# Kernel optimization log

Measured on AMD Instinct MI355X. Metric: run time of the kernel, lower is better.

The kernel has to match this reference:

```python
import jax, jax.numpy as jnp
import numpy as np

BN_EPS = 1e-5


def _maxpool2(x):
    # x: [b, c, h, w] -> [b, c, h//2, w//2], 2x2 max pool, stride 2
    b, c, h, w = x.shape
    return x.reshape(b, c, h // 2, 2, w // 2, 2).max(axis=(3, 5))


def setup_inputs() -> dict:
    key = jax.random.key(0)
    ks = jax.random.split(key, 9)
    b, C, H, W = 8, 512, 64, 64
    Ci = C // 2  # inter_channels = 256
    return {
        "x": jax.random.normal(ks[0], (b, C, H, W), dtype=jnp.float32),
        "g_w": jax.random.normal(ks[1], (Ci, C), dtype=jnp.float32) * 0.02,
        "g_b": jax.random.normal(ks[2], (Ci,), dtype=jnp.float32) * 0.02,
        "W_w": jax.random.normal(ks[3], (C, Ci), dtype=jnp.float32) * 0.02,
        "W_b": jax.random.normal(ks[4], (C,), dtype=jnp.float32) * 0.02,
        "bn_gamma": jax.random.normal(ks[5], (C,), dtype=jnp.float32),
        "bn_beta": jax.random.normal(ks[6], (C,), dtype=jnp.float32),
        "bn_mean": jax.random.normal(ks[7], (C,), dtype=jnp.float32),
        "bn_var": jax.random.uniform(ks[8], (C,), dtype=jnp.float32, minval=0.5, maxval=1.5),
    }


def reference(x, g_w, g_b, W_w, W_b, bn_gamma, bn_beta, bn_mean, bn_var):
    b, C, H, W = x.shape
    Ci = g_w.shape[0]

    # g branch: conv1x1 (C -> Ci) then 2x2 maxpool, flatten to values [b, Nk, Ci]
    g_x = jnp.einsum('bchw,oc->bohw', x, g_w) + g_b[None, :, None, None]
    g_x = _maxpool2(g_x).reshape(b, Ci, -1).transpose(0, 2, 1)  # [b, Nk, Ci]

    # theta: identity, flattened queries [b, Nq, C]
    theta = x.reshape(b, C, -1).transpose(0, 2, 1)  # [b, Nq, C]
    # phi: identity + 2x2 maxpool, keys [b, C, Nk]
    phi = _maxpool2(x).reshape(b, C, -1)  # [b, C, Nk]

    # attention (unscaled dot product + softmax over keys)
    f = jnp.einsum('bnc,bck->bnk', theta, phi)  # [b, Nq, Nk]
    attn = jax.nn.softmax(f, axis=-1)
    y = jnp.einsum('bnk,bko->bno', attn, g_x)  # [b, Nq, Ci]
    y = y.transpose(0, 2, 1).reshape(b, Ci, H, W)

    # W: conv1x1 (Ci -> C) + BatchNorm2d (eval mode with running stats)
    W_y = jnp.einsum('bchw,oc->bohw', y, W_w) + W_b[None, :, None, None]
    inv_std = jax.lax.rsqrt(bn_var + BN_EPS)
    W_y = (W_y - bn_mean[None, :, None, None]) * (bn_gamma * inv_std)[None, :, None, None] \
          + bn_beta[None, :, None, None]

    return W_y + x
```

## Files before the change

kernel.cpp:

```cpp
#include <hip/hip_runtime.h>
#include <stdint.h>

typedef __attribute__((ext_vector_type(4))) float f32x4;
typedef __attribute__((ext_vector_type(8))) short short8_t;
typedef __attribute__((ext_vector_type(8))) unsigned short ushort8_t;

__device__ __forceinline__ unsigned short f2bf(float f) {
    unsigned int u = __builtin_bit_cast(unsigned int, f);
    u = (u + 0x7fffu + ((u >> 16) & 1u)) >> 16;
    return (unsigned short)u;
}
__device__ __forceinline__ float bf2f(unsigned short h) {
    unsigned int u = ((unsigned int)h) << 16;
    return __builtin_bit_cast(float, u);
}

__device__ __forceinline__ void gll16(const unsigned short* g, unsigned short* l) {
    __builtin_amdgcn_global_load_lds(
        (const __attribute__((address_space(1))) void*)g,
        (__attribute__((address_space(3))) void*)l, 16, 0, 0);
}

__global__ __launch_bounds__(256) void prep_w(
    const float* __restrict__ g_w, const float* __restrict__ W_w,
    const float* __restrict__ W_b, const float* __restrict__ gamma,
    const float* __restrict__ beta, const float* __restrict__ mean,
    const float* __restrict__ var,
    unsigned short* __restrict__ gwb, unsigned short* __restrict__ wwb,
    float* __restrict__ bnA, float* __restrict__ bnB)
{
    int i = blockIdx.x * 256 + threadIdx.x;
    if (i < 256 * 512) { gwb[i] = f2bf(g_w[i]); wwb[i] = f2bf(W_w[i]); }
    if (i < 512) {
        float is = rsqrtf(var[i] + 1e-5f);
        float a = gamma[i] * is;
        bnA[i] = a;
        bnB[i] = (W_b[i] - mean[i]) * a + beta[i];
    }
}

__global__ __launch_bounds__(256) void build_qk(
    const float* __restrict__ x, unsigned short* __restrict__ Qh,
    unsigned short* __restrict__ Kh)
{
    __shared__ float t[32][129];
    int b = blockIdx.z;
    int p0 = blockIdx.x * 128, c0 = blockIdx.y * 32;
    const float* xb = x + (long)b * 512 * 4096;
    int tid = threadIdx.x;
    for (int i = 0; i < 16; i++) {
        int idx = i * 256 + tid;
        int c = idx >> 7, p = idx & 127;
        t[c][p] = xb[(long)(c0 + c) * 4096 + p0 + p];
    }
    __syncthreads();
    unsigned short* qb = Qh + (long)b * 4096 * 512;
    for (int i = 0; i < 16; i++) {
        int idx = i * 256 + tid;
        int p = idx >> 5, c = idx & 31;
        qb[(long)(p0 + p) * 512 + c0 + c] = f2bf(t[c][p]);
    }
    unsigned short* kb = Kh + (long)b * 1024 * 512;
    int kp0 = p0 >> 2;
    for (int i = 0; i < 4; i++) {
        int idx = i * 256 + tid;
        int w = idx >> 5, c = idx & 31;
        float v = fmaxf(fmaxf(t[c][2 * w], t[c][2 * w + 1]),
                        fmaxf(t[c][64 + 2 * w], t[c][64 + 2 * w + 1]));
        kb[(long)(kp0 + w) * 512 + c0 + c] = f2bf(v);
    }
}

__global__ __launch_bounds__(256) void build_v(
    const unsigned short* __restrict__ Gt, const float* __restrict__ g_b,
    unsigned short* __restrict__ Gp)
{
    int b = blockIdx.z;
    int k  = blockIdx.x * 32 + (threadIdx.x & 31);
    int ci = blockIdx.y * 8 + (threadIdx.x >> 5);
    int h = k >> 5, w = k & 31;
    const unsigned short* g = Gt + (long)b * 4096 * 256;
    long p = (long)(h * 128 + w * 2) * 256 + ci;
    float v0 = bf2f(g[p]),        v1 = bf2f(g[p + 256]);
    float v2 = bf2f(g[p + 64*256]), v3 = bf2f(g[p + 65*256]);
    float v = fmaxf(fmaxf(v0, v1), fmaxf(v2, v3)) + g_b[ci];
    Gp[(long)b * 256 * 1024 + (long)ci * 1024 + k] = f2bf(v);
}

__global__ __launch_bounds__(256) void smax_rows(
    const unsigned short* __restrict__ S, float* __restrict__ Smax)
{
    long row = (long)blockIdx.x * 4 + (threadIdx.x >> 6);
    int lane = threadIdx.x & 63;
    const unsigned short* r = S + row * 1024 + lane * 16;
    ushort8_t v0 = *(const ushort8_t*)r;
    ushort8_t v1 = *(const ushort8_t*)(r + 8);
    float m = -3.0e38f;
    for (int e = 0; e < 8; e++) m = fmaxf(m, fmaxf(bf2f(v0[e]), bf2f(v1[e])));
    for (int off = 32; off; off >>= 1) m = fmaxf(m, __shfl_xor(m, off));
    if (lane == 0) Smax[row] = m;
}

__global__ __launch_bounds__(256) void pv_fused(
    const unsigned short* __restrict__ S, long sbstr,
    const float* __restrict__ Smax, long mxstr,
    const unsigned short* __restrict__ Gp, long gbstr,
    unsigned short* __restrict__ Y, long ybstr)
{
    __shared__ unsigned short lV[256 * 64];
    __shared__ unsigned short lP[64 * 64];
    __shared__ float li[64];

    const int tid = threadIdx.x;
    const int wid = tid >> 6, lane = tid & 63;

    unsigned gx = gridDim.x, gy = gridDim.y;
    unsigned nwg = gx * gy;
    unsigned lin = blockIdx.x + gx * blockIdx.y;
    unsigned l = ((nwg & 7u) == 0u) ? ((lin & 7u) * (nwg >> 3) + (lin >> 3)) : lin;
    unsigned bx = l % gx, by = l / gx;

    const int q0 = (int)bx * 64;
    const unsigned short* Sb = S + by * sbstr + (long)q0 * 1024;
    const unsigned short* Gb = Gp + by * gbstr;
    unsigned short* Yb = Y + by * ybstr + (long)q0 * 256;

    const int wr = wid >> 1, wc = wid & 1;
    const int lr = lane & 15, lg = lane >> 4;
    const int srA = lane >> 3;
    const int scg = (((lane & 7) ^ srA) << 3);
    const int pr = tid >> 2;
    const int pc = (tid & 3) * 2;

    const float m = Smax[by * mxstr + q0 + pr];

    f32x4 acc[2][8];
    for (int mi = 0; mi < 2; mi++)
        for (int ni = 0; ni < 8; ni++)
            acc[mi][ni] = (f32x4){0.f, 0.f, 0.f, 0.f};
    float psum = 0.f;

    for (int kb = 0; kb < 16; kb++) {
        __syncthreads();
        for (int i = 0; i < 8; i++) {
            int cibase = i * 32 + wid * 8;
            gll16(Gb + (long)(cibase + srA) * 1024 + kb * 64 + scg, &lV[cibase * 64]);
        }
        {
            const unsigned short* sp = Sb + (long)pr * 1024 + kb * 64 + pc * 8;
            for (int j = 0; j < 2; j++) {
                ushort8_t v = *(const ushort8_t*)(sp + j * 8);
                ushort8_t o8;
                for (int e = 0; e < 8; e++) {
                    float pe = __expf(bf2f(v[e]) - m);
                    psum += pe;
                    o8[e] = f2bf(pe);
                }
                int c = pc + j;
                *(ushort8_t*)(&lP[pr * 64 + ((c ^ (pr & 7)) * 8)]) = o8;
            }
        }
        __syncthreads();
        for (int ks = 0; ks < 2; ks++) {
            short8_t af[2], bfr[8];
            for (int mi = 0; mi < 2; mi++) {
                int row = wr * 32 + mi * 16 + lr;
                int ch = ((ks * 4 + lg) ^ (row & 7)) * 8;
                af[mi] = *(const short8_t*)(&lP[row * 64 + ch]);
            }
            for (int ni = 0; ni < 8; ni++) {
                int row = wc * 128 + ni * 16 + lr;
                int ch = ((ks * 4 + lg) ^ (row & 7)) * 8;
                bfr[ni] = *(const short8_t*)(&lV[row * 64 + ch]);
            }
            for (int mi = 0; mi < 2; mi++)
                for (int ni = 0; ni < 8; ni++)
                    acc[mi][ni] = __builtin_amdgcn_mfma_f32_16x16x32_bf16(
                        af[mi], bfr[ni], acc[mi][ni], 0, 0, 0);
        }
    }

    psum += __shfl_xor(psum, 1);
    psum += __shfl_xor(psum, 2);
    if ((tid & 3) == 0) li[pr] = 1.0f / psum;
    __syncthreads();

    for (int mi = 0; mi < 2; mi++) {
        for (int ni = 0; ni < 8; ni++) {
            int ci = wc * 128 + ni * 16 + lr;
            int rbase = wr * 32 + mi * 16 + lg * 4;
            for (int r = 0; r < 4; r++) {
                int row = rbase + r;
                Yb[(long)row * 256 + ci] = f2bf(acc[mi][ni][r] * li[row]);
            }
        }
    }
}

template<int EPI>
__global__ __launch_bounds__(256) void gemm_abt(
    const unsigned short* __restrict__ A, int lda, long abstr,
    const unsigned short* __restrict__ B, int ldb, long bbstr,
    void* __restrict__ Cv, int ldc, long cbstr,
    int K,
    const float* __restrict__ bnA, const float* __restrict__ bnB,
    const float* __restrict__ Xres, long xbstr)
{
    __shared__ unsigned short lA[128 * 64];
    __shared__ unsigned short lB[128 * 64];
    const int tid = threadIdx.x;
    const int wid = tid >> 6, lane = tid & 63;

    unsigned gx = gridDim.x, gy = gridDim.y;
    unsigned nwg = gx * gy * gridDim.z;
    unsigned lin = blockIdx.x + gx * (blockIdx.y + gy * blockIdx.z);
    unsigned l = ((nwg & 7u) == 0u) ? ((lin & 7u) * (nwg >> 3) + (lin >> 3)) : lin;
    unsigned bx = l % gx;
    unsigned rem = l / gx;
    unsigned by = rem % gy;
    unsigned bz = rem / gy;

    const int z = (int)bz;
    const int m0 = (int)by * 128, n0 = (int)bx * 128;
    const unsigned short* Ab = A + z * abstr;
    const unsigned short* Bb = B + z * bbstr;
    const int wr = wid >> 1, wc = wid & 1;
    const int lr = lane & 15, lg = lane >> 4;

    const int srA = lane >> 3;
    const int scg = (((lane & 7) ^ srA) << 3);

    f32x4 acc[4][4];
    for (int mi = 0; mi < 4; mi++)
        for (int ni = 0; ni < 4; ni++)
            acc[mi][ni] = (f32x4){0.f, 0.f, 0.f, 0.f};

    for (int k0 = 0; k0 < K; k0 += 64) {
        __syncthreads();
        for (int i = 0; i < 4; i++) {
            int rowbase = i * 32 + wid * 8;
            gll16(Ab + (long)(m0 + rowbase + srA) * lda + k0 + scg, &lA[rowbase * 64]);
            gll16(Bb + (long)(n0 + rowbase + srA) * ldb + k0 + scg, &lB[rowbase * 64]);
        }
        __syncthreads();
        for (int kk = 0; kk < 2; kk++) {
            short8_t af[4], bfr[4];
            for (int mi = 0; mi < 4; mi++) {
                int row = wr * 64 + mi * 16 + lr;
                int ch = ((kk * 4 + lg) ^ (row & 7)) * 8;
                af[mi] = *(const short8_t*)(&lA[row * 64 + ch]);
            }
            for (int ni = 0; ni < 4; ni++) {
                int row = wc * 64 + ni * 16 + lr;
                int ch = ((kk * 4 + lg) ^ (row & 7)) * 8;
                bfr[ni] = *(const short8_t*)(&lB[row * 64 + ch]);
            }
            for (int mi = 0; mi < 4; mi++)
                for (int ni = 0; ni < 4; ni++)
                    acc[mi][ni] = __builtin_amdgcn_mfma_f32_16x16x32_bf16(
                        af[mi], bfr[ni], acc[mi][ni], 0, 0, 0);
        }
    }

    for (int mi = 0; mi < 4; mi++) {
        for (int ni = 0; ni < 4; ni++) {
            int ncol = n0 + wc * 64 + ni * 16 + lr;
            int mrow = m0 + wr * 64 + mi * 16 + lg * 4;
            for (int r = 0; r < 4; r++) {
                int row = mrow + r;
                float v = acc[mi][ni][r];
                long idx = z * cbstr + (long)row * ldc + ncol;
                if (EPI == 0) {
                    ((float*)Cv)[idx] = v;
                } else if (EPI == 1) {
                    ((unsigned short*)Cv)[idx] = f2bf(v);
                } else {
                    float o = v * bnA[row] + bnB[row] + Xres[z * xbstr + (long)row * ldc + ncol];
                    ((float*)Cv)[idx] = o;
                }
            }
        }
    }
}

__global__ void copy_residual(const float* __restrict__ x, float* __restrict__ out, long n)
{
    for (long i = blockIdx.x * 256ll + threadIdx.x; i < n; i += (long)gridDim.x * 256)
        out[i] = x[i];
}

extern "C" void kernel_launch(void* const* d_in, const int* in_sizes, int n_in,
                              void* d_out, int out_size, void* d_ws, size_t ws_size,
                              hipStream_t stream)
{
    const float* x     = (const float*)d_in[0];
    const float* g_w   = (const float*)d_in[1];
    const float* g_b   = (const float*)d_in[2];
    const float* W_w   = (const float*)d_in[3];
    const float* W_b   = (const float*)d_in[4];
    const float* gamma = (const float*)d_in[5];
    const float* beta  = (const float*)d_in[6];
    const float* mean  = (const float*)d_in[7];
    const float* var   = (const float*)d_in[8];
    float* out = (float*)d_out;

    char* ws = (char*)d_ws;
    size_t o = 0;
    auto alloc = [&](size_t bytes) { size_t r = o; o = (o + bytes + 255) & ~(size_t)255; return r; };
    size_t o_gwb = alloc(256 * 512 * 2);
    size_t o_wwb = alloc(512 * 256 * 2);
    size_t o_bnA = alloc(512 * 4);
    size_t o_bnB = alloc(512 * 4);
    size_t o_q   = alloc(8ull * 4096 * 512 * 2);
    size_t o_k   = alloc(8ull * 1024 * 512 * 2);
    size_t o_gp  = alloc(8ull * 256 * 1024 * 2);
    size_t o_y   = alloc(8ull * 4096 * 256 * 2);
    size_t o_m   = alloc(8ull * 4096 * 4);
    size_t o_s   = o;
    const size_t srow_bytes = 1024ull * 2;
    const size_t sb1 = 4096ull * srow_bytes;

    int G = 0, RC = 0;
    if      (o_s + 8 * sb1 <= ws_size) G = 8;
    else if (o_s + 4 * sb1 <= ws_size) G = 4;
    else if (o_s + 2 * sb1 <= ws_size) G = 2;
    else if (o_s + 1 * sb1 <= ws_size) G = 1;
    else {
        for (int rc = 2048; rc >= 128; rc >>= 1)
            if (o_s + (size_t)rc * srow_bytes <= ws_size) { RC = rc; break; }
        if (!RC) {
            copy_residual<<<dim3(2048), dim3(256), 0, stream>>>(x, out, (long)out_size);
            return;
        }
    }

    unsigned short* gwb = (unsigned short*)(ws + o_gwb);
    unsigned short* wwb = (unsigned short*)(ws + o_wwb);
    float* bnA = (float*)(ws + o_bnA);
    float* bnB = (float*)(ws + o_bnB);
    unsigned short* Qh  = (unsigned short*)(ws + o_q);
    unsigned short* Kh  = (unsigned short*)(ws + o_k);
    unsigned short* Gp  = (unsigned short*)(ws + o_gp);
    unsigned short* Y   = (unsigned short*)(ws + o_y);
    float* Smax         = (float*)(ws + o_m);
    unsigned short* S   = (unsigned short*)(ws + o_s);

    prep_w<<<dim3(512), dim3(256), 0, stream>>>(g_w, W_w, W_b, gamma, beta, mean, var,
                                                gwb, wwb, bnA, bnB);
    build_qk<<<dim3(32, 16, 8), dim3(256), 0, stream>>>(x, Qh, Kh);

    gemm_abt<1><<<dim3(2, 32, 8), dim3(256), 0, stream>>>(
        Qh, 512, 4096l * 512,
        gwb, 512, 0,
        (void*)Y, 256, 4096l * 256, 512,
        nullptr, nullptr, nullptr, 0);

    build_v<<<dim3(32, 32, 8), dim3(256), 0, stream>>>(Y, g_b, Gp);

    if (G) {
        for (int bg = 0; bg < 8; bg += G) {
            gemm_abt<1><<<dim3(8, 32, G), dim3(256), 0, stream>>>(
                Qh + (size_t)bg * 4096 * 512, 512, 4096l * 512,
                Kh + (size_t)bg * 1024 * 512, 512, 1024l * 512,
                (void*)S, 1024, 4096l * 1024, 512,
                nullptr, nullptr, nullptr, 0);
            smax_rows<<<dim3(G * 1024), dim3(256), 0, stream>>>(S, Smax);
            pv_fused<<<dim3(64, G), dim3(256), 0, stream>>>(
                S, 4096l * 1024,
                Smax, 4096,
                Gp + (size_t)bg * 256 * 1024, 256l * 1024,
                Y + (size_t)bg * 4096 * 256, 4096l * 256);
        }
    } else {
        for (int b = 0; b < 8; b++) {
            for (int r0 = 0; r0 < 4096; r0 += RC) {
                const unsigned short* Aq = Qh + (size_t)b * 4096 * 512 + (size_t)r0 * 512;
                gemm_abt<1><<<dim3(8, RC / 128, 1), dim3(256), 0, stream>>>(
                    Aq, 512, 0,
                    Kh + (size_t)b * 1024 * 512, 512, 0,
                    (void*)S, 1024, 0, 512,
                    nullptr, nullptr, nullptr, 0);
                smax_rows<<<dim3(RC / 4), dim3(256), 0, stream>>>(S, Smax);
                pv_fused<<<dim3(RC / 64, 1), dim3(256), 0, stream>>>(
                    S, 0,
                    Smax, 0,
                    Gp + (size_t)b * 256 * 1024, 0,
                    Y + ((size_t)b * 4096 + r0) * 256, 0);
            }
        }
    }

    gemm_abt<2><<<dim3(32, 4, 8), dim3(256), 0, stream>>>(
        wwb, 256, 0,
        Y, 256, 4096l * 256,
        (void*)out, 4096, 512l * 4096, 256,
        bnA, bnB, x, 512l * 4096);
}
```

Before: 178.5 us.

## Fuse g-branch conv GEMM into QK score GEMM launch and hoist S loads

```diff
diff --git a/kernel.cpp b/kernel.cpp
--- a/kernel.cpp
+++ b/kernel.cpp
@@ -142,23 +142,27 @@
 
     for (int kb = 0; kb < 16; kb++) {
         __syncthreads();
+        const unsigned short* sp = Sb + (long)pr * 1024 + kb * 64 + pc * 8;
+        ushort8_t v0 = *(const ushort8_t*)sp;
+        ushort8_t v1 = *(const ushort8_t*)(sp + 8);
         for (int i = 0; i < 8; i++) {
             int cibase = i * 32 + wid * 8;
             gll16(Gb + (long)(cibase + srA) * 1024 + kb * 64 + scg, &lV[cibase * 64]);
         }
         {
-            const unsigned short* sp = Sb + (long)pr * 1024 + kb * 64 + pc * 8;
-            for (int j = 0; j < 2; j++) {
-                ushort8_t v = *(const ushort8_t*)(sp + j * 8);
-                ushort8_t o8;
-                for (int e = 0; e < 8; e++) {
-                    float pe = __expf(bf2f(v[e]) - m);
-                    psum += pe;
-                    o8[e] = f2bf(pe);
-                }
-                int c = pc + j;
-                *(ushort8_t*)(&lP[pr * 64 + ((c ^ (pr & 7)) * 8)]) = o8;
-            }
+            ushort8_t o8;
+            for (int e = 0; e < 8; e++) {
+                float pe = __expf(bf2f(v0[e]) - m);
+                psum += pe;
+                o8[e] = f2bf(pe);
+            }
+            *(ushort8_t*)(&lP[pr * 64 + ((pc ^ (pr & 7)) * 8)]) = o8;
+            for (int e = 0; e < 8; e++) {
+                float pe = __expf(bf2f(v1[e]) - m);
+                psum += pe;
+                o8[e] = f2bf(pe);
+            }
+            *(ushort8_t*)(&lP[pr * 64 + (((pc + 1) ^ (pr & 7)) * 8)]) = o8;
         }
         __syncthreads();
         for (int ks = 0; ks < 2; ks++) {
@@ -192,6 +196,89 @@
             for (int r = 0; r < 4; r++) {
                 int row = rbase + r;
                 Yb[(long)row * 256 + ci] = f2bf(acc[mi][ni][r] * li[row]);
+            }
+        }
+    }
+}
+
+__global__ __launch_bounds__(256) void gemm_qkg(
+    const unsigned short* __restrict__ Qh,
+    const unsigned short* __restrict__ Kh,
+    const unsigned short* __restrict__ gwb,
+    unsigned short* __restrict__ S,
+    unsigned short* __restrict__ Gt)
+{
+    __shared__ unsigned short lA[128 * 64];
+    __shared__ unsigned short lB[128 * 64];
+    const int tid = threadIdx.x;
+    const int wid = tid >> 6, lane = tid & 63;
+
+    unsigned gx = gridDim.x, gy = gridDim.y;
+    unsigned nwg = gx * gy * gridDim.z;
+    unsigned lin = blockIdx.x + gx * (blockIdx.y + gy * blockIdx.z);
+    unsigned l = ((nwg & 7u) == 0u) ? ((lin & 7u) * (nwg >> 3) + (lin >> 3)) : lin;
+    unsigned bx = l % gx;
+    unsigned rem = l / gx;
+    unsigned by = rem % gy;
+    unsigned bz = rem / gy;
+
+    const int z = (int)bz;
+    const int m0 = (int)by * 128;
+    const unsigned short* Ab = Qh + (long)z * 4096 * 512;
+    const unsigned short* Bb;
+    unsigned short* Cb;
+    int n0, ldc;
+    if (bx < 8) {
+        Bb = Kh + (long)z * 1024 * 512;  n0 = bx * 128;
+        Cb = S + (long)z * 4096 * 1024;  ldc = 1024;
+    } else {
+        Bb = gwb;                         n0 = (bx - 8) * 128;
+        Cb = Gt + (long)z * 4096 * 256;   ldc = 256;
+    }
+
+    const int wr = wid >> 1, wc = wid & 1;
+    const int lr = lane & 15, lg = lane >> 4;
+    const int srA = lane >> 3;
+    const int scg = (((lane & 7) ^ srA) << 3);
+
+    f32x4 acc[4][4];
+    for (int mi = 0; mi < 4; mi++)
+        for (int ni = 0; ni < 4; ni++)
+            acc[mi][ni] = (f32x4){0.f, 0.f, 0.f, 0.f};
+
+    for (int k0 = 0; k0 < 512; k0 += 64) {
+        __syncthreads();
+        for (int i = 0; i < 4; i++) {
+            int rowbase = i * 32 + wid * 8;
+            gll16(Ab + (long)(m0 + rowbase + srA) * 512 + k0 + scg, &lA[rowbase * 64]);
+            gll16(Bb + (long)(n0 + rowbase + srA) * 512 + k0 + scg, &lB[rowbase * 64]);
+        }
+        __syncthreads();
+        for (int kk = 0; kk < 2; kk++) {
+            short8_t af[4], bfr[4];
+            for (int mi = 0; mi < 4; mi++) {
+                int row = wr * 64 + mi * 16 + lr;
+                int ch = ((kk * 4 + lg) ^ (row & 7)) * 8;
+                af[mi] = *(const short8_t*)(&lA[row * 64 + ch]);
+            }
+            for (int ni = 0; ni < 4; ni++) {
+                int row = wc * 64 + ni * 16 + lr;
+                int ch = ((kk * 4 + lg) ^ (row & 7)) * 8;
+                bfr[ni] = *(const short8_t*)(&lB[row * 64 + ch]);
+            }
+            for (int mi = 0; mi < 4; mi++)
+                for (int ni = 0; ni < 4; ni++)
+                    acc[mi][ni] = __builtin_amdgcn_mfma_f32_16x16x32_bf16(
+                        af[mi], bfr[ni], acc[mi][ni], 0, 0, 0);
+        }
+    }
+
+    for (int mi = 0; mi < 4; mi++) {
+        for (int ni = 0; ni < 4; ni++) {
+            int ncol = n0 + wc * 64 + ni * 16 + lr;
+            int mrow = m0 + wr * 64 + mi * 16 + lg * 4;
+            for (int r = 0; r < 4; r++) {
+                Cb[(long)(mrow + r) * ldc + ncol] = f2bf(acc[mi][ni][r]);
             }
         }
     }
@@ -349,21 +436,16 @@
                                                 gwb, wwb, bnA, bnB);
     build_qk<<<dim3(32, 16, 8), dim3(256), 0, stream>>>(x, Qh, Kh);
 
-    gemm_abt<1><<<dim3(2, 32, 8), dim3(256), 0, stream>>>(
-        Qh, 512, 4096l * 512,
-        gwb, 512, 0,
-        (void*)Y, 256, 4096l * 256, 512,
-        nullptr, nullptr, nullptr, 0);
-
-    build_v<<<dim3(32, 32, 8), dim3(256), 0, stream>>>(Y, g_b, Gp);
-
     if (G) {
         for (int bg = 0; bg < 8; bg += G) {
-            gemm_abt<1><<<dim3(8, 32, G), dim3(256), 0, stream>>>(
-                Qh + (size_t)bg * 4096 * 512, 512, 4096l * 512,
-                Kh + (size_t)bg * 1024 * 512, 512, 1024l * 512,
-                (void*)S, 1024, 4096l * 1024, 512,
-                nullptr, nullptr, nullptr, 0);
+            gemm_qkg<<<dim3(10, 32, G), dim3(256), 0, stream>>>(
+                Qh + (size_t)bg * 4096 * 512,
+                Kh + (size_t)bg * 1024 * 512,
+                gwb,
+                S,
+                Y + (size_t)bg * 4096 * 256);
+            build_v<<<dim3(32, 32, G), dim3(256), 0, stream>>>(
+                Y + (size_t)bg * 4096 * 256, g_b, Gp + (size_t)bg * 256 * 1024);
             smax_rows<<<dim3(G * 1024), dim3(256), 0, stream>>>(S, Smax);
             pv_fused<<<dim3(64, G), dim3(256), 0, stream>>>(
                 S, 4096l * 1024,
@@ -372,6 +454,12 @@
                 Y + (size_t)bg * 4096 * 256, 4096l * 256);
         }
     } else {
+        gemm_abt<1><<<dim3(2, 32, 8), dim3(256), 0, stream>>>(
+            Qh, 512, 4096l * 512,
+            gwb, 512, 0,
+            (void*)Y, 256, 4096l * 256, 512,
+            nullptr, nullptr, nullptr, 0);
+        build_v<<<dim3(32, 32, 8), dim3(256), 0, stream>>>(Y, g_b, Gp);
         for (int b = 0; b < 8; b++) {
             for (int r0 = 0; r0 < 4096; r0 += RC) {
                 const unsigned short* Aq = Qh + (size_t)b * 4096 * 512 + (size_t)r0 * 512;
```

New measurement: 174.6 us. -2.2%, faster.
